# Kernel optimization log

Measured on AMD Instinct MI355X. Metric: run time of the kernel, lower is better.

Reference implementation:

```python
import jax, jax.numpy as jnp
import numpy as np

T, B, H, NH = 256, 64, 768, 12
HD = H // NH


def setup_inputs() -> dict:
    key = jax.random.key(0)
    ks = jax.random.split(key, 24)
    stdv = 1.0 / np.sqrt(H)
    u = lambda k, shape: jax.random.uniform(k, shape, jnp.float32, -stdv, stdv)
    return {
        "question": jax.random.normal(ks[0], (1, B, H), jnp.float32),
        "answer": jax.random.normal(ks[1], (1, B, H), jnp.float32),
        "x": jax.random.normal(ks[2], (T, B, H), jnp.float32),
        "ping": jax.random.randint(ks[3], (B, T), 0, T, jnp.int32),
        "h0": jax.random.normal(ks[4], (1, B, H), jnp.float32),
        "c0": jax.random.normal(ks[5], (1, B, H), jnp.float32),
        # SQACILSTMCell parameters (num_layers=1)
        "Wqh": u(ks[6], (H, 4 * H)), "bqh": u(ks[7], (4 * H,)),
        "Wah": u(ks[8], (H, 4 * H)), "bah": u(ks[9], (4 * H,)),
        "Wih": u(ks[10], (H, 4 * H)), "bih": u(ks[11], (4 * H,)),
        "Whh": u(ks[12], (H, 4 * H)), "bhh": u(ks[13], (4 * H,)),
        # BertSelfAttention parameters
        "Wq": u(ks[14], (H, H)), "bq": u(ks[15], (H,)),
        "Wk": u(ks[16], (H, H)), "bk": u(ks[17], (H,)),
        "Wv": u(ks[18], (H, H)), "bv": u(ks[19], (H,)),
        # fusion linear (ci_mode='all'): Linear(2H -> H), stored as [2H, H]
        "Wfuse": u(ks[20], (2 * H, H)), "bfuse": u(ks[21], (H,)),
    }


def reference(question, answer, x, ping, h0, c0,
              Wqh, bqh, Wah, bah, Wih, bih, Whh, bhh,
              Wq, bq, Wk, bk, Wv, bv, Wfuse, bfuse):
    Tn, Bn, Hn = x.shape
    scale = 1.0 / np.sqrt(HD)
    barange = jnp.arange(Bn)
    # q/a contributions are time-invariant: precompute once
    base = (question[0] @ Wqh + bqh) + (answer[0] @ Wah + bah) + bih + bhh  # [B,4H]

    def attn2(pair):  # pair: [B,2,H] -> fused [B,H]
        def heads(y):
            return y.reshape(Bn, 2, NH, HD).transpose(0, 2, 1, 3)  # [B,NH,2,HD]
        q = heads(pair @ Wq + bq)
        k = heads(pair @ Wk + bk)
        v = heads(pair @ Wv + bv)
        s = jnp.einsum('bhqd,bhkd->bhqk', q, k) * scale
        p = jax.nn.softmax(s, axis=-1)
        ctx = jnp.einsum('bhqk,bhkd->bhqd', p, v).transpose(0, 2, 1, 3).reshape(Bn, 2, Hn)
        # ci_mode='all': concat both tokens then linear 2H->H
        return jnp.concatenate([ctx[:, 0], ctx[:, 1]], axis=-1) @ Wfuse + bfuse

    def step(carry, t):
        h_prev, c_prev, inputs = carry
        pt = ping[:, t]  # [B]
        left = inputs[jnp.clip(pt - 1, 0, Tn - 1), barange]  # [B,H] data-dependent gather
        right = inputs[t]  # [B,H]
        fused = attn2(jnp.stack([left, right], axis=1))
        newv = jnp.where(((pt > 0) & (t > 0))[:, None], fused, right)
        inputs = inputs.at[t].set(newv)  # refactoring persists across steps
        gates = base + newv @ Wih + h_prev @ Whh  # [B,4H]
        i, f, g, o = jnp.split(gates, 4, axis=1)
        c = jax.nn.sigmoid(f) * c_prev + jax.nn.sigmoid(i) * jnp.tanh(g)
        h = jax.nn.sigmoid(o) * jnp.tanh(c)
        return (h, c, inputs), h

    (hT, cT, _), h_all = jax.lax.scan(step, (h0[0], c0[0], x), jnp.arange(Tn))
    # matches torch return: (h[:, -1], (h[-1], c[-1])) with num_layers=1
    return h_all, hT[None], cT[None]
```

## Files before the change

### kernel.cpp

```cpp
#include <hip/hip_runtime.h>
#include <cstdint>
#include <cstddef>


#define T_   256
#define B_   64
#define NBLK 72
#define NTHR 256
#define GRIDTH (NBLK*NTHR)
#define HALL 12582912

typedef __attribute__((ext_vector_type(8))) short short8;
typedef __attribute__((ext_vector_type(4))) float f4;
typedef unsigned long long u64t;
typedef unsigned short u16t;
typedef unsigned int u32t;

struct Params {
  const float* question; const float* answer; const float* x; const int* ping;
  const float* h0; const float* c0;
  const float* Wqh; const float* bqh; const float* Wah; const float* bah;
  const float* Wih; const float* bih; const float* Whh; const float* bhh;
  const float* Wq;  const float* bq;  const float* Wk;  const float* bk;
  const float* Wv;  const float* bv;  const float* Wfuse; const float* bfuse;
  float* out;
  u32t* flags; u32t* gen;
  u16t* Wqkv_s; u16t* Whhih_s; u16t* Wfuse_s; u16t* Wcomb_s; u16t* Wfuse_bf;
  float* base; float* gatesHX; u16t* ctxb; u16t* hB; float* cbuf; float* bfW;
  u16t* xB;
};

__device__ __forceinline__ u16t f2b(float f){
  union { float f; u32t u; } a; a.f = f;
  u32t u = a.u;
  u32t r = u + 0x7FFFu + ((u >> 16) & 1u);
  return (u16t)(r >> 16);
}
__device__ __forceinline__ float b2f(u16t u){
  union { u32t u; float f; } a; a.u = ((u32t)u) << 16; return a.f;
}
__device__ __forceinline__ u64t pack4f(float a, float b, float c, float d){
  return (u64t)f2b(a) | ((u64t)f2b(b)<<16) | ((u64t)f2b(c)<<32) | ((u64t)f2b(d)<<48);
}
__device__ __forceinline__ float sigm(float x){ return 1.0f/(1.0f+__expf(-x)); }
__device__ __forceinline__ float tanh_(float x){ return 2.0f/(1.0f+__expf(-2.0f*x)) - 1.0f; }
__device__ __forceinline__ f4 mfma16(short8 a, short8 b, f4 c){
  return __builtin_amdgcn_mfma_f32_16x16x32_bf16(a, b, c, 0, 0, 0);
}
__device__ __forceinline__ float wsum(float x){
  #pragma unroll
  for (int off = 32; off > 0; off >>= 1) x += __shfl_xor(x, off, 64);
  return x;
}

__device__ __forceinline__ void cldx4_8(f4&d0,f4&d1,f4&d2,f4&d3,f4&d4,f4&d5,f4&d6,f4&d7,
  const void*a0,const void*a1,const void*a2,const void*a3,
  const void*a4,const void*a5,const void*a6,const void*a7){
  asm volatile(
    "global_load_dwordx4 %0, %8, off sc0 sc1\n\t"
    "global_load_dwordx4 %1, %9, off sc0 sc1\n\t"
    "global_load_dwordx4 %2, %10, off sc0 sc1\n\t"
    "global_load_dwordx4 %3, %11, off sc0 sc1\n\t"
    "global_load_dwordx4 %4, %12, off sc0 sc1\n\t"
    "global_load_dwordx4 %5, %13, off sc0 sc1\n\t"
    "global_load_dwordx4 %6, %14, off sc0 sc1\n\t"
    "global_load_dwordx4 %7, %15, off sc0 sc1\n\t"
    "s_waitcnt vmcnt(0)"
    : "=&v"(d0),"=&v"(d1),"=&v"(d2),"=&v"(d3),"=&v"(d4),"=&v"(d5),"=&v"(d6),"=&v"(d7)
    : "v"(a0),"v"(a1),"v"(a2),"v"(a3),"v"(a4),"v"(a5),"v"(a6),"v"(a7));
}
__device__ __forceinline__ void cldx4_4(f4&d0,f4&d1,f4&d2,f4&d3,
  const void*a0,const void*a1,const void*a2,const void*a3){
  asm volatile(
    "global_load_dwordx4 %0, %4, off sc0 sc1\n\t"
    "global_load_dwordx4 %1, %5, off sc0 sc1\n\t"
    "global_load_dwordx4 %2, %6, off sc0 sc1\n\t"
    "global_load_dwordx4 %3, %7, off sc0 sc1\n\t"
    "s_waitcnt vmcnt(0)"
    : "=&v"(d0),"=&v"(d1),"=&v"(d2),"=&v"(d3)
    : "v"(a0),"v"(a1),"v"(a2),"v"(a3));
}
__device__ __forceinline__ void cldd8(float&d0,float&d1,float&d2,float&d3,float&d4,float&d5,float&d6,float&d7,
  const float*a0,const float*a1,const float*a2,const float*a3,
  const float*a4,const float*a5,const float*a6,const float*a7){
  asm volatile(
    "global_load_dword %0, %8, off sc0 sc1\n\t"
    "global_load_dword %1, %9, off sc0 sc1\n\t"
    "global_load_dword %2, %10, off sc0 sc1\n\t"
    "global_load_dword %3, %11, off sc0 sc1\n\t"
    "global_load_dword %4, %12, off sc0 sc1\n\t"
    "global_load_dword %5, %13, off sc0 sc1\n\t"
    "global_load_dword %6, %14, off sc0 sc1\n\t"
    "global_load_dword %7, %15, off sc0 sc1\n\t"
    "s_waitcnt vmcnt(0)"
    : "=&v"(d0),"=&v"(d1),"=&v"(d2),"=&v"(d3),"=&v"(d4),"=&v"(d5),"=&v"(d6),"=&v"(d7)
    : "v"(a0),"v"(a1),"v"(a2),"v"(a3),"v"(a4),"v"(a5),"v"(a6),"v"(a7));
}

__device__ __forceinline__ void cstf(float* p, float v){
  __hip_atomic_store(p, v, __ATOMIC_RELAXED, __HIP_MEMORY_SCOPE_AGENT);
}
__device__ __forceinline__ void cst32(u32t* p, u32t v){
  __hip_atomic_store(p, v, __ATOMIC_RELAXED, __HIP_MEMORY_SCOPE_AGENT);
}

__device__ __forceinline__ void aput16(u16t* As, int rowu16, int m, int cc, f4 v){
  int slot = (cc & ~7) | ((cc ^ m) & 7);
  *(f4*)(As + m*rowu16 + slot*8) = v;
}
__device__ __forceinline__ short8 afrag(const u16t* As, int rowu16, int m, int kb, int q4){
  int c = kb*4 + q4;
  int phys = (c & ~7) | ((c ^ m) & 7);
  return *(const short8*)(As + m*rowu16 + phys*8);
}

__device__ __forceinline__ void gsync(u32t* flags, u32t* gen, u32t e){
  asm volatile("s_waitcnt vmcnt(0) lgkmcnt(0)" ::: "memory");
  __syncthreads();
  if (blockIdx.x == 0){
    if (threadIdx.x > 0 && threadIdx.x < NBLK){
      while (__hip_atomic_load(flags + threadIdx.x*32, __ATOMIC_RELAXED, __HIP_MEMORY_SCOPE_AGENT) < e) ;
    }
    __syncthreads();
    if (threadIdx.x == 0)
      __hip_atomic_store(gen, e, __ATOMIC_RELAXED, __HIP_MEMORY_SCOPE_AGENT);
  } else {
    if (threadIdx.x == 0){
      __hip_atomic_store(flags + blockIdx.x*32, e, __ATOMIC_RELAXED, __HIP_MEMORY_SCOPE_AGENT);
      while (__hip_atomic_load(gen, __ATOMIC_RELAXED, __HIP_MEMORY_SCOPE_AGENT) < e) ;
    }
  }
  __builtin_amdgcn_fence(__ATOMIC_ACQUIRE, "workgroup");
  __syncthreads();
}

__launch_bounds__(NTHR, 1)
__global__ void sqac_kernel(Params p){
  extern __shared__ u16t As[];
  __shared__ u16t qkvs[64*192];
  __shared__ int anyX;
  const int tid0 = threadIdx.x;
  const int blk  = blockIdx.x;
  const int tid  = blk*NTHR + tid0;
  const int lane = tid0 & 63;
  const int wv   = tid0 >> 6;
  const int c16  = lane & 15, q4 = lane >> 4;
  u32t e = 0;

  {
    for (int idx = tid; idx < 12288; idx += GRIDTH){
      f4 h = *(const f4*)(p.h0 + idx*4);
      *(u64t*)(p.hB + idx*4) = pack4f(h.x, h.y, h.z, h.w);
      *(f4*)(p.cbuf + idx*4) = *(const f4*)(p.c0 + idx*4);
    }
    for (int idx = tid; idx < 3145728; idx += GRIDTH){
      f4 v = *(const f4*)(p.x + (size_t)idx*4);
      *(u64t*)(p.xB + (size_t)idx*4) = pack4f(v.x, v.y, v.z, v.w);
    }
    for (int idx = tid; idx < 221184; idx += GRIDTH){
      int l = idx & 63, g2 = idx >> 6;
      int ntl = g2 % 12, kb = (g2/12) % 24, h = g2/288;
      int k0 = kb*32 + ((l>>4)<<3);
      int nl = ntl*16 + (l&15);
      const float* s; int col;
      if (nl < 64){ s = p.Wq; col = h*64 + nl; }
      else if (nl < 128){ s = p.Wk; col = h*64 + nl - 64; }
      else { s = p.Wv; col = h*64 + nl - 128; }
      union { u16t a[8]; short8 v; } t8;
      #pragma unroll
      for (int j = 0; j < 8; j++) t8.a[j] = f2b(s[(size_t)(k0+j)*768 + col]);
      *(short8*)(p.Wqkv_s + (size_t)idx*8) = t8.v;
    }
    for (int idx = tid; idx < 589824; idx += GRIDTH){
      int l = idx & 63, g2 = idx >> 6;
      int nb = g2 % 192, kb2 = g2 / 192;
      int n  = nb*16 + (l&15);
      int kl = (kb2 % 24)*32 + ((l>>4)<<3);
      const float* s = (kb2 < 24) ? p.Whh : p.Wih;
      union { u16t a[8]; short8 v; } t8;
      #pragma unroll
      for (int j = 0; j < 8; j++) t8.a[j] = f2b(s[(size_t)(kl+j)*3072 + n]);
      *(short8*)(p.Whhih_s + (size_t)idx*8) = t8.v;
    }
    for (int idx = tid; idx < 147456; idx += GRIDTH){
      int l = idx & 63, g2 = idx >> 6;
      int nb = g2 % 48, kb = g2 / 48;
      int n  = nb*16 + (l&15);
      int k0 = kb*32 + ((l>>4)<<3);
      union { u16t a[8]; short8 v; } t8;
      #pragma unroll
      for (int j = 0; j < 8; j++) t8.a[j] = f2b(p.Wfuse[(size_t)(k0+j)*768 + n]);
      *(short8*)(p.Wfuse_s + (size_t)idx*8) = t8.v;
    }
    for (int idx = tid; idx < 294912; idx += GRIDTH){
      f4 v = *(const f4*)(p.Wfuse + idx*4);
      *(u64t*)(p.Wfuse_bf + idx*4) = pack4f(v.x, v.y, v.z, v.w);
    }
    for (int w = tid; w < 24576; w += GRIDTH){
      int bg = w / 3072, n = w - bg*3072;
      float acc[8];
      #pragma unroll
      for (int bi = 0; bi < 8; bi++) acc[bi] = 0.f;
      for (int k = 0; k < 768; k++){
        float wq = p.Wqh[(size_t)k*3072 + n];
        float wa = p.Wah[(size_t)k*3072 + n];
        #pragma unroll
        for (int bi = 0; bi < 8; bi++){
          int b = bg*8 + bi;
          acc[bi] += p.question[b*768 + k]*wq + p.answer[b*768 + k]*wa;
        }
      }
      float bias = p.bqh[n] + p.bah[n] + p.bih[n] + p.bhh[n];
      #pragma unroll
      for (int bi = 0; bi < 8; bi++)
        p.base[(size_t)(bg*8+bi)*3072 + n] = acc[bi] + bias;
    }
    for (int n = tid; n < 3072; n += GRIDTH){
      float a = 0.f;
      for (int k = 0; k < 768; k++) a += p.bfuse[k]*p.Wih[(size_t)k*3072 + n];
      p.bfW[n] = a;
    }
  }
  __threadfence();
  e++; gsync(p.flags, p.gen, e);

  {
    int w = tid >> 6;
    int mt = w % 96, ntg = w / 96;
    for (int nt = ntg*64; nt < ntg*64 + 64; nt++){
      f4 acc = {0.f,0.f,0.f,0.f};
      for (int kb = 0; kb < 24; kb++){
        short8 af = *(const short8*)(p.Wfuse_bf + (size_t)(mt*16 + c16)*768 + kb*32 + q4*8);
        short8 bf = *(const short8*)(p.Whhih_s + ((size_t)((24+kb)*192 + nt))*512 + lane*8);
        acc = mfma16(af, bf, acc);
      }
      #pragma unroll
      for (int r = 0; r < 4; r++){
        int k1 = mt*16 + q4*4 + r;
        p.Wcomb_s[((size_t)((k1>>5)*192 + nt))*512 + (size_t)((((k1>>3)&3)*16 + c16)*8 + (k1&7))] = f2b(acc[r]);
      }
    }
  }
  __threadfence();
  e++; gsync(p.flags, p.gen, e);

  for (int t = 0; t < T_; t++){

    if (blk < 24){
      int h, bh;
      if (blk < 16){ h = blk & 7; bh = blk >> 3; }
      else { int l2 = blk - 16; h = 8 + (l2 & 3); bh = l2 >> 2; }
      {
        int m = tid0 >> 2, j = tid0 & 3;
        int b = bh*32 + (m & 31);
        int st;
        if (m < 32){ int pt = p.ping[b*T_ + t]; st = pt - 1; if (st < 0) st = 0; if (st > T_-1) st = T_-1; }
        else st = t;
        const f4* src = (const f4*)(p.xB + ((size_t)(st*64 + b))*768);
        #pragma unroll
        for (int g = 0; g < 3; g++){
          f4 d0,d1,d2,d3,d4,d5,d6,d7;
          int c0 = j + 32*g;
          cldx4_8(d0,d1,d2,d3,d4,d5,d6,d7,
                  src+c0,    src+c0+ 4, src+c0+ 8, src+c0+12,
                  src+c0+16, src+c0+20, src+c0+24, src+c0+28);
          aput16(As,768,m,c0,    d0); aput16(As,768,m,c0+ 4,d1);
          aput16(As,768,m,c0+ 8, d2); aput16(As,768,m,c0+12,d3);
          aput16(As,768,m,c0+16, d4); aput16(As,768,m,c0+20,d5);
          aput16(As,768,m,c0+24, d6); aput16(As,768,m,c0+28,d7);
        }
      }
      __syncthreads();
      f4 acc[3][4];
      #pragma unroll
      for (int i = 0; i < 3; i++)
        #pragma unroll
        for (int mt = 0; mt < 4; mt++) acc[i][mt] = f4{0.f,0.f,0.f,0.f};
      for (int kb = 0; kb < 24; kb++){
        short8 af[4];
        #pragma unroll
        for (int mt = 0; mt < 4; mt++) af[mt] = afrag(As, 768, mt*16 + c16, kb, q4);
        #pragma unroll
        for (int i = 0; i < 3; i++){
          short8 bf = *(const short8*)(p.Wqkv_s + ((size_t)((h*24 + kb)*12 + wv*3 + i))*512 + lane*8);
          #pragma unroll
          for (int mt = 0; mt < 4; mt++) acc[i][mt] = mfma16(af[mt], bf, acc[i][mt]);
        }
      }
      #pragma unroll
      for (int i = 0; i < 3; i++){
        int nl = (wv*3 + i)*16 + c16;
        float bias = (nl < 64) ? p.bq[h*64+nl] : (nl < 128 ? p.bk[h*64+nl-64] : p.bv[h*64+nl-128]);
        #pragma unroll
        for (int mt = 0; mt < 4; mt++)
          #pragma unroll
          for (int r = 0; r < 4; r++)
            qkvs[(mt*16 + q4*4 + r)*192 + nl] = f2b(acc[i][mt][r] + bias);
      }
      __syncthreads();
      for (int pi = 0; pi < 8; pi++){
        int bi = wv*8 + pi;
        const u16t* L = qkvs + bi*192;
        const u16t* R = qkvs + (32+bi)*192;
        float ql = b2f(L[lane]), kl = b2f(L[64+lane]), vl = b2f(L[128+lane]);
        float qr = b2f(R[lane]), kr = b2f(R[64+lane]), vr = b2f(R[128+lane]);
        float sll = wsum(ql*kl)*0.125f, slr = wsum(ql*kr)*0.125f;
        float srl = wsum(qr*kl)*0.125f, srr = wsum(qr*kr)*0.125f;
        float ml = fmaxf(sll, slr), mr = fmaxf(srl, srr);
        float ell = __expf(sll-ml), elr = __expf(slr-ml);
        float erl = __expf(srl-mr), err = __expf(srr-mr);
        float il = 1.0f/(ell+elr), ir = 1.0f/(erl+err);
        float cl = (ell*il)*vl + (elr*il)*vr;
        float cr = (erl*ir)*vl + (err*ir)*vr;
        float cl2 = __shfl_xor(cl, 1), cr2 = __shfl_xor(cr, 1);
        if (!(lane & 1)){
          int b = bh*32 + bi;
          cst32((u32t*)(p.ctxb + (size_t)b*1536 + h*64 + lane),
                (u32t)f2b(cl) | ((u32t)f2b(cl2) << 16));
          cst32((u32t*)(p.ctxb + (size_t)b*1536 + 768 + h*64 + lane),
                (u32t)f2b(cr) | ((u32t)f2b(cr2) << 16));
        }
      }
    } else {
      const int local = blk - 24, mh = local / 24, ng = local % 24;
      const int b0 = mh*32;
      if (tid0 == 0) anyX = 0;
      __syncthreads();
      {
        int m = tid0 >> 3, j = tid0 & 7;
        int b = b0 + m;
        int pt = p.ping[b*T_ + t];
        bool cond = (pt > 0) && (t > 0);
        const f4* hsrc = (const f4*)(p.hB + (size_t)b*768);
        {
          f4 d0,d1,d2,d3,d4,d5,d6,d7;
          cldx4_8(d0,d1,d2,d3,d4,d5,d6,d7,
                  hsrc+j,    hsrc+j+ 8, hsrc+j+16, hsrc+j+24,
                  hsrc+j+32, hsrc+j+40, hsrc+j+48, hsrc+j+56);
          aput16(As,1536,m,j,    d0); aput16(As,1536,m,j+ 8,d1);
          aput16(As,1536,m,j+16, d2); aput16(As,1536,m,j+24,d3);
          aput16(As,1536,m,j+32, d4); aput16(As,1536,m,j+40,d5);
          aput16(As,1536,m,j+48, d6); aput16(As,1536,m,j+56,d7);
          f4 e0,e1,e2,e3;
          cldx4_4(e0,e1,e2,e3, hsrc+j+64, hsrc+j+72, hsrc+j+80, hsrc+j+88);
          aput16(As,1536,m,j+64, e0); aput16(As,1536,m,j+72,e1);
          aput16(As,1536,m,j+80, e2); aput16(As,1536,m,j+88,e3);
        }
        if (cond){
          #pragma unroll
          for (int i = 0; i < 12; i++) aput16(As,1536,m,96 + j + 8*i, f4{0.f,0.f,0.f,0.f});
        } else {
          if (j == 0) anyX = 1;
          const f4* xsrc = (const f4*)(p.xB + ((size_t)(t*64 + b))*768);
          f4 d0,d1,d2,d3,d4,d5,d6,d7;
          cldx4_8(d0,d1,d2,d3,d4,d5,d6,d7,
                  xsrc+j,    xsrc+j+ 8, xsrc+j+16, xsrc+j+24,
                  xsrc+j+32, xsrc+j+40, xsrc+j+48, xsrc+j+56);
          aput16(As,1536,m,96+j,    d0); aput16(As,1536,m,96+j+ 8,d1);
          aput16(As,1536,m,96+j+16, d2); aput16(As,1536,m,96+j+24,d3);
          aput16(As,1536,m,96+j+32, d4); aput16(As,1536,m,96+j+40,d5);
          aput16(As,1536,m,96+j+48, d6); aput16(As,1536,m,96+j+56,d7);
          f4 e0,e1,e2,e3;
          cldx4_4(e0,e1,e2,e3, xsrc+j+64, xsrc+j+72, xsrc+j+80, xsrc+j+88);
          aput16(As,1536,m,96+j+64, e0); aput16(As,1536,m,96+j+72,e1);
          aput16(As,1536,m,96+j+80, e2); aput16(As,1536,m,96+j+88,e3);
        }
      }
      __syncthreads();
      const int kbmax = anyX ? 48 : 24;
      f4 acc[2][2];
      #pragma unroll
      for (int i = 0; i < 2; i++)
        #pragma unroll
        for (int mt = 0; mt < 2; mt++) acc[i][mt] = f4{0.f,0.f,0.f,0.f};
      for (int kb = 0; kb < kbmax; kb++){
        short8 af[2];
        #pragma unroll
        for (int mt = 0; mt < 2; mt++) af[mt] = afrag(As, 1536, mt*16 + c16, kb, q4);
        #pragma unroll
        for (int i = 0; i < 2; i++){
          int nt = ng*8 + wv*2 + i;
          short8 bf = *(const short8*)(p.Whhih_s + ((size_t)(kb*192 + nt))*512 + lane*8);
          #pragma unroll
          for (int mt = 0; mt < 2; mt++) acc[i][mt] = mfma16(af[mt], bf, acc[i][mt]);
        }
      }
      #pragma unroll
      for (int i = 0; i < 2; i++){
        int n = (ng*8 + wv*2 + i)*16 + c16;
        #pragma unroll
        for (int mt = 0; mt < 2; mt++)
          #pragma unroll
          for (int r = 0; r < 4; r++){
            int b = b0 + mt*16 + q4*4 + r;
            cstf(p.gatesHX + (size_t)b*3072 + n, acc[i][mt][r]);
          }
      }
    }
    e++; gsync(p.flags, p.gen, e);

    if (blk < 48){
      const int mh = blk / 24, jjg = blk % 24;
      const int b0 = mh*32;
      {
        int m = tid0 >> 3, j = tid0 & 7;
        const f4* src = (const f4*)(p.ctxb + (size_t)(b0+m)*1536);
        #pragma unroll
        for (int g = 0; g < 3; g++){
          f4 d0,d1,d2,d3,d4,d5,d6,d7;
          int c0 = j + 64*g;
          cldx4_8(d0,d1,d2,d3,d4,d5,d6,d7,
                  src+c0,    src+c0+ 8, src+c0+16, src+c0+24,
                  src+c0+32, src+c0+40, src+c0+48, src+c0+56);
          aput16(As,1536,m,c0,    d0); aput16(As,1536,m,c0+ 8,d1);
          aput16(As,1536,m,c0+16, d2); aput16(As,1536,m,c0+24,d3);
          aput16(As,1536,m,c0+32, d4); aput16(As,1536,m,c0+40,d5);
          aput16(As,1536,m,c0+48, d6); aput16(As,1536,m,c0+56,d7);
        }
      }
      __syncthreads();
      const int jjt = jjg*2 + (wv & 1), mt = wv >> 1;
      const int jj = jjt*16 + c16;
      float gx[16];
      {
        const float* a[16];
        #pragma unroll
        for (int r = 0; r < 4; r++){
          int b = b0 + mt*16 + q4*4 + r;
          size_t g0 = (size_t)b*3072 + jj;
          a[r*4+0] = p.gatesHX + g0;        a[r*4+1] = p.gatesHX + g0 + 768;
          a[r*4+2] = p.gatesHX + g0 + 1536; a[r*4+3] = p.gatesHX + g0 + 2304;
        }
        cldd8(gx[0],gx[1],gx[2],gx[3],gx[4],gx[5],gx[6],gx[7],
              a[0],a[1],a[2],a[3],a[4],a[5],a[6],a[7]);
        cldd8(gx[8],gx[9],gx[10],gx[11],gx[12],gx[13],gx[14],gx[15],
              a[8],a[9],a[10],a[11],a[12],a[13],a[14],a[15]);
      }
      f4 acc[4];
      #pragma unroll
      for (int g = 0; g < 4; g++) acc[g] = f4{0.f,0.f,0.f,0.f};
      for (int kb = 0; kb < 48; kb++){
        short8 af = afrag(As, 1536, mt*16 + c16, kb, q4);
        #pragma unroll
        for (int g = 0; g < 4; g++){
          short8 bf = *(const short8*)(p.Wcomb_s + ((size_t)(kb*192 + g*48 + jjt))*512 + lane*8);
          acc[g] = mfma16(af, bf, acc[g]);
        }
      }
      float bfw[4];
      #pragma unroll
      for (int g = 0; g < 4; g++) bfw[g] = p.bfW[g*768 + jj];
      #pragma unroll
      for (int r = 0; r < 4; r++){
        int b = b0 + mt*16 + q4*4 + r;
        int pt = p.ping[b*T_ + t];
        bool cond = (pt > 0) && (t > 0);
        size_t g0 = (size_t)b*3072 + jj;
        float gi = p.base[g0]      + gx[r*4+0];
        float gf = p.base[g0+768]  + gx[r*4+1];
        float gg = p.base[g0+1536] + gx[r*4+2];
        float go = p.base[g0+2304] + gx[r*4+3];
        if (cond){
          gi += acc[0][r] + bfw[0]; gf += acc[1][r] + bfw[1];
          gg += acc[2][r] + bfw[2]; go += acc[3][r] + bfw[3];
        }
        float co = p.cbuf[b*768 + jj];
        float cn = sigm(gf)*co + sigm(gi)*tanh_(gg);
        float hh = sigm(go)*tanh_(cn);
        p.out[((size_t)(t*64 + b))*768 + jj] = hh;
        p.cbuf[b*768 + jj] = cn;
        float hp = __shfl_xor(hh, 1);
        if (!(c16 & 1))
          cst32((u32t*)(p.hB + (size_t)b*768 + jj), (u32t)f2b(hh) | ((u32t)f2b(hp) << 16));
        if (t == T_-1){
          p.out[HALL + b*768 + jj] = hh;
          p.out[HALL + 49152 + b*768 + jj] = cn;
        }
      }
    } else {
      const int local = blk - 48;
      int ng, mh;
      if (local < 16){ ng = local & 7; mh = local >> 3; }
      else { int l2 = local - 16; ng = 8 + (l2 & 3); mh = l2 >> 2; }
      const int b0 = mh*32;
      {
        int m = tid0 >> 3, j = tid0 & 7;
        const f4* src = (const f4*)(p.ctxb + (size_t)(b0+m)*1536);
        #pragma unroll
        for (int g = 0; g < 3; g++){
          f4 d0,d1,d2,d3,d4,d5,d6,d7;
          int c0 = j + 64*g;
          cldx4_8(d0,d1,d2,d3,d4,d5,d6,d7,
                  src+c0,    src+c0+ 8, src+c0+16, src+c0+24,
                  src+c0+32, src+c0+40, src+c0+48, src+c0+56);
          aput16(As,1536,m,c0,    d0); aput16(As,1536,m,c0+ 8,d1);
          aput16(As,1536,m,c0+16, d2); aput16(As,1536,m,c0+24,d3);
          aput16(As,1536,m,c0+32, d4); aput16(As,1536,m,c0+40,d5);
          aput16(As,1536,m,c0+48, d6); aput16(As,1536,m,c0+56,d7);
        }
      }
      __syncthreads();
      const int nt = ng*4 + wv;
      f4 acc[2];
      #pragma unroll
      for (int mt = 0; mt < 2; mt++) acc[mt] = f4{0.f,0.f,0.f,0.f};
      for (int kb = 0; kb < 48; kb++){
        short8 bf = *(const short8*)(p.Wfuse_s + ((size_t)(kb*48 + nt))*512 + lane*8);
        #pragma unroll
        for (int mt = 0; mt < 2; mt++){
          short8 af = afrag(As, 1536, mt*16 + c16, kb, q4);
          acc[mt] = mfma16(af, bf, acc[mt]);
        }
      }
      const int n = nt*16 + c16;
      const float bias = p.bfuse[n];
      #pragma unroll
      for (int mt = 0; mt < 2; mt++)
        #pragma unroll
        for (int r = 0; r < 4; r++){
          int b = b0 + mt*16 + q4*4 + r;
          int pt = p.ping[b*T_ + t];
          float v = acc[mt][r] + bias;
          float v2 = __shfl_xor(v, 1);
          if ((pt > 0) && (t > 0) && !(c16 & 1))
            cst32((u32t*)(p.xB + ((size_t)(t*64 + b))*768 + n),
                  (u32t)f2b(v) | ((u32t)f2b(v2) << 16));
        }
    }
    e++; gsync(p.flags, p.gen, e);
  }
}

extern "C" void kernel_launch(void* const* d_in, const int* in_sizes, int n_in,
                              void* d_out, int out_size, void* d_ws, size_t ws_size,
                              hipStream_t stream)
{
  (void)in_sizes; (void)n_in; (void)out_size; (void)ws_size;
  char* ws = (char*)d_ws;
  size_t off = 0;
  auto take = [&](size_t bytes)->void*{
    void* ptr = ws + off;
    off += (bytes + 255) & ~(size_t)255;
    return ptr;
  };

  Params p;
  p.question = (const float*)d_in[0];
  p.answer   = (const float*)d_in[1];
  p.x        = (const float*)d_in[2];
  p.ping     = (const int*)d_in[3];
  p.h0  = (const float*)d_in[4];  p.c0  = (const float*)d_in[5];
  p.Wqh = (const float*)d_in[6];  p.bqh = (const float*)d_in[7];
  p.Wah = (const float*)d_in[8];  p.bah = (const float*)d_in[9];
  p.Wih = (const float*)d_in[10]; p.bih = (const float*)d_in[11];
  p.Whh = (const float*)d_in[12]; p.bhh = (const float*)d_in[13];
  p.Wq  = (const float*)d_in[14]; p.bq  = (const float*)d_in[15];
  p.Wk  = (const float*)d_in[16]; p.bk  = (const float*)d_in[17];
  p.Wv  = (const float*)d_in[18]; p.bv  = (const float*)d_in[19];
  p.Wfuse = (const float*)d_in[20]; p.bfuse = (const float*)d_in[21];
  p.out = (float*)d_out;

  u32t* sync = (u32t*)take(16384);
  p.flags = sync;
  p.gen   = sync + 3072;

  p.Wqkv_s   = (u16t*)take((size_t)221184*16);
  p.Whhih_s  = (u16t*)take((size_t)589824*16);
  p.Wfuse_s  = (u16t*)take((size_t)147456*16);
  p.Wcomb_s  = (u16t*)take((size_t)589824*16);
  p.Wfuse_bf = (u16t*)take((size_t)1536*768*2);
  p.base     = (float*)take((size_t)64*3072*4);
  p.gatesHX  = (float*)take((size_t)64*3072*4);
  p.ctxb     = (u16t*)take((size_t)64*1536*2);
  p.hB       = (u16t*)take((size_t)64*768*2);
  p.cbuf     = (float*)take((size_t)64*768*4);
  p.bfW      = (float*)take((size_t)3072*4);
  p.xB       = (u16t*)take((size_t)12582912*2);

  hipFuncSetAttribute(reinterpret_cast<const void*>(sqac_kernel),
                      hipFuncAttributeMaxDynamicSharedMemorySize, 98304);
  hipMemsetAsync(sync, 0, 16384, stream);
  hipLaunchKernelGGL(sqac_kernel, dim3(NBLK), dim3(NTHR), 98304, stream, p);
}
```

Before: 17.11 ms.

## Double threads per block with split-K wave pairs and sleep in grid barrier

Raises the block size from 256 to 512 threads and reassigns the new waves in each phase of the persistent recurrent kernel. The QKV and gates GEMMs split work along M, and the fuse and Wcomb GEMMs split K in half, with partial sums reduced through a new shared-memory buffer. Global-to-LDS staging is rewritten for the wider blocks, and the grid-barrier spin loops now call s_sleep to cut memory polling pressure. The aim is more latency hiding per step on the serial time loop, at the cost of extra block-level syncs, reduction traffic and possible barrier wake-up delay.

```diff
diff --git a/kernel.cpp b/kernel.cpp
--- a/kernel.cpp
+++ b/kernel.cpp
@@ -6,7 +6,7 @@
 #define T_   256
 #define B_   64
 #define NBLK 72
-#define NTHR 256
+#define NTHR 512
 #define GRIDTH (NBLK*NTHR)
 #define HALL 12582912
 
@@ -69,6 +69,20 @@
     : "=&v"(d0),"=&v"(d1),"=&v"(d2),"=&v"(d3),"=&v"(d4),"=&v"(d5),"=&v"(d6),"=&v"(d7)
     : "v"(a0),"v"(a1),"v"(a2),"v"(a3),"v"(a4),"v"(a5),"v"(a6),"v"(a7));
 }
+__device__ __forceinline__ void cldx4_6(f4&d0,f4&d1,f4&d2,f4&d3,f4&d4,f4&d5,
+  const void*a0,const void*a1,const void*a2,const void*a3,
+  const void*a4,const void*a5){
+  asm volatile(
+    "global_load_dwordx4 %0, %6, off sc0 sc1\n\t"
+    "global_load_dwordx4 %1, %7, off sc0 sc1\n\t"
+    "global_load_dwordx4 %2, %8, off sc0 sc1\n\t"
+    "global_load_dwordx4 %3, %9, off sc0 sc1\n\t"
+    "global_load_dwordx4 %4, %10, off sc0 sc1\n\t"
+    "global_load_dwordx4 %5, %11, off sc0 sc1\n\t"
+    "s_waitcnt vmcnt(0)"
+    : "=&v"(d0),"=&v"(d1),"=&v"(d2),"=&v"(d3),"=&v"(d4),"=&v"(d5)
+    : "v"(a0),"v"(a1),"v"(a2),"v"(a3),"v"(a4),"v"(a5));
+}
 __device__ __forceinline__ void cldx4_4(f4&d0,f4&d1,f4&d2,f4&d3,
   const void*a0,const void*a1,const void*a2,const void*a3){
   asm volatile(
@@ -119,7 +133,8 @@
   __syncthreads();
   if (blockIdx.x == 0){
     if (threadIdx.x > 0 && threadIdx.x < NBLK){
-      while (__hip_atomic_load(flags + threadIdx.x*32, __ATOMIC_RELAXED, __HIP_MEMORY_SCOPE_AGENT) < e) ;
+      while (__hip_atomic_load(flags + threadIdx.x*32, __ATOMIC_RELAXED, __HIP_MEMORY_SCOPE_AGENT) < e)
+        __builtin_amdgcn_s_sleep(1);
     }
     __syncthreads();
     if (threadIdx.x == 0)
@@ -127,7 +142,8 @@
   } else {
     if (threadIdx.x == 0){
       __hip_atomic_store(flags + blockIdx.x*32, e, __ATOMIC_RELAXED, __HIP_MEMORY_SCOPE_AGENT);
-      while (__hip_atomic_load(gen, __ATOMIC_RELAXED, __HIP_MEMORY_SCOPE_AGENT) < e) ;
+      while (__hip_atomic_load(gen, __ATOMIC_RELAXED, __HIP_MEMORY_SCOPE_AGENT) < e)
+        __builtin_amdgcn_s_sleep(1);
     }
   }
   __builtin_amdgcn_fence(__ATOMIC_ACQUIRE, "workgroup");
@@ -138,6 +154,7 @@
 __global__ void sqac_kernel(Params p){
   extern __shared__ u16t As[];
   __shared__ u16t qkvs[64*192];
+  __shared__ float red[4][64][16];
   __shared__ int anyX;
   const int tid0 = threadIdx.x;
   const int blk  = blockIdx.x;
@@ -227,7 +244,7 @@
   {
     int w = tid >> 6;
     int mt = w % 96, ntg = w / 96;
-    for (int nt = ntg*64; nt < ntg*64 + 64; nt++){
+    for (int nt = ntg*32; nt < ntg*32 + 32; nt++){
       f4 acc = {0.f,0.f,0.f,0.f};
       for (int kb = 0; kb < 24; kb++){
         short8 af = *(const short8*)(p.Wfuse_bf + (size_t)(mt*16 + c16)*768 + kb*32 + q4*8);
@@ -251,55 +268,59 @@
       if (blk < 16){ h = blk & 7; bh = blk >> 3; }
       else { int l2 = blk - 16; h = 8 + (l2 & 3); bh = l2 >> 2; }
       {
-        int m = tid0 >> 2, j = tid0 & 3;
+        int m = tid0 >> 3, j = tid0 & 7;
         int b = bh*32 + (m & 31);
         int st;
         if (m < 32){ int pt = p.ping[b*T_ + t]; st = pt - 1; if (st < 0) st = 0; if (st > T_-1) st = T_-1; }
         else st = t;
         const f4* src = (const f4*)(p.xB + ((size_t)(st*64 + b))*768);
-        #pragma unroll
-        for (int g = 0; g < 3; g++){
-          f4 d0,d1,d2,d3,d4,d5,d6,d7;
-          int c0 = j + 32*g;
-          cldx4_8(d0,d1,d2,d3,d4,d5,d6,d7,
-                  src+c0,    src+c0+ 4, src+c0+ 8, src+c0+12,
-                  src+c0+16, src+c0+20, src+c0+24, src+c0+28);
-          aput16(As,768,m,c0,    d0); aput16(As,768,m,c0+ 4,d1);
-          aput16(As,768,m,c0+ 8, d2); aput16(As,768,m,c0+12,d3);
-          aput16(As,768,m,c0+16, d4); aput16(As,768,m,c0+20,d5);
-          aput16(As,768,m,c0+24, d6); aput16(As,768,m,c0+28,d7);
-        }
-      }
-      __syncthreads();
-      f4 acc[3][4];
+        f4 d0,d1,d2,d3,d4,d5,d6,d7;
+        cldx4_8(d0,d1,d2,d3,d4,d5,d6,d7,
+                src+j,    src+j+ 8, src+j+16, src+j+24,
+                src+j+32, src+j+40, src+j+48, src+j+56);
+        aput16(As,768,m,j,    d0); aput16(As,768,m,j+ 8,d1);
+        aput16(As,768,m,j+16, d2); aput16(As,768,m,j+24,d3);
+        aput16(As,768,m,j+32, d4); aput16(As,768,m,j+40,d5);
+        aput16(As,768,m,j+48, d6); aput16(As,768,m,j+56,d7);
+        f4 e0,e1,e2,e3;
+        cldx4_4(e0,e1,e2,e3, src+j+64, src+j+72, src+j+80, src+j+88);
+        aput16(As,768,m,j+64, e0); aput16(As,768,m,j+72,e1);
+        aput16(As,768,m,j+80, e2); aput16(As,768,m,j+88,e3);
+      }
+      __syncthreads();
+      const int wvL = wv & 3, mh2 = wv >> 2;
+      f4 acc[3][2];
       #pragma unroll
       for (int i = 0; i < 3; i++)
         #pragma unroll
-        for (int mt = 0; mt < 4; mt++) acc[i][mt] = f4{0.f,0.f,0.f,0.f};
+        for (int mtl = 0; mtl < 2; mtl++) acc[i][mtl] = f4{0.f,0.f,0.f,0.f};
       for (int kb = 0; kb < 24; kb++){
-        short8 af[4];
-        #pragma unroll
-        for (int mt = 0; mt < 4; mt++) af[mt] = afrag(As, 768, mt*16 + c16, kb, q4);
+        short8 af[2];
+        #pragma unroll
+        for (int mtl = 0; mtl < 2; mtl++)
+          af[mtl] = afrag(As, 768, (mh2*2 + mtl)*16 + c16, kb, q4);
         #pragma unroll
         for (int i = 0; i < 3; i++){
-          short8 bf = *(const short8*)(p.Wqkv_s + ((size_t)((h*24 + kb)*12 + wv*3 + i))*512 + lane*8);
-          #pragma unroll
-          for (int mt = 0; mt < 4; mt++) acc[i][mt] = mfma16(af[mt], bf, acc[i][mt]);
+          short8 bf = *(const short8*)(p.Wqkv_s + ((size_t)((h*24 + kb)*12 + wvL*3 + i))*512 + lane*8);
+          #pragma unroll
+          for (int mtl = 0; mtl < 2; mtl++) acc[i][mtl] = mfma16(af[mtl], bf, acc[i][mtl]);
         }
       }
       #pragma unroll
       for (int i = 0; i < 3; i++){
-        int nl = (wv*3 + i)*16 + c16;
+        int nl = (wvL*3 + i)*16 + c16;
         float bias = (nl < 64) ? p.bq[h*64+nl] : (nl < 128 ? p.bk[h*64+nl-64] : p.bv[h*64+nl-128]);
         #pragma unroll
-        for (int mt = 0; mt < 4; mt++)
+        for (int mtl = 0; mtl < 2; mtl++){
+          int mt = mh2*2 + mtl;
           #pragma unroll
           for (int r = 0; r < 4; r++)
-            qkvs[(mt*16 + q4*4 + r)*192 + nl] = f2b(acc[i][mt][r] + bias);
-      }
-      __syncthreads();
-      for (int pi = 0; pi < 8; pi++){
-        int bi = wv*8 + pi;
+            qkvs[(mt*16 + q4*4 + r)*192 + nl] = f2b(acc[i][mtl][r] + bias);
+        }
+      }
+      __syncthreads();
+      for (int pi = 0; pi < 4; pi++){
+        int bi = wv*4 + pi;
         const u16t* L = qkvs + bi*192;
         const u16t* R = qkvs + (32+bi)*192;
         float ql = b2f(L[lane]), kl = b2f(L[64+lane]), vl = b2f(L[128+lane]);
@@ -327,74 +348,56 @@
       if (tid0 == 0) anyX = 0;
       __syncthreads();
       {
-        int m = tid0 >> 3, j = tid0 & 7;
+        int m = tid0 >> 4, j = tid0 & 15;
         int b = b0 + m;
         int pt = p.ping[b*T_ + t];
         bool cond = (pt > 0) && (t > 0);
         const f4* hsrc = (const f4*)(p.hB + (size_t)b*768);
         {
-          f4 d0,d1,d2,d3,d4,d5,d6,d7;
-          cldx4_8(d0,d1,d2,d3,d4,d5,d6,d7,
-                  hsrc+j,    hsrc+j+ 8, hsrc+j+16, hsrc+j+24,
-                  hsrc+j+32, hsrc+j+40, hsrc+j+48, hsrc+j+56);
-          aput16(As,1536,m,j,    d0); aput16(As,1536,m,j+ 8,d1);
-          aput16(As,1536,m,j+16, d2); aput16(As,1536,m,j+24,d3);
-          aput16(As,1536,m,j+32, d4); aput16(As,1536,m,j+40,d5);
-          aput16(As,1536,m,j+48, d6); aput16(As,1536,m,j+56,d7);
-          f4 e0,e1,e2,e3;
-          cldx4_4(e0,e1,e2,e3, hsrc+j+64, hsrc+j+72, hsrc+j+80, hsrc+j+88);
-          aput16(As,1536,m,j+64, e0); aput16(As,1536,m,j+72,e1);
-          aput16(As,1536,m,j+80, e2); aput16(As,1536,m,j+88,e3);
+          f4 d0,d1,d2,d3,d4,d5;
+          cldx4_6(d0,d1,d2,d3,d4,d5,
+                  hsrc+j, hsrc+j+16, hsrc+j+32, hsrc+j+48, hsrc+j+64, hsrc+j+80);
+          aput16(As,1536,m,j,    d0); aput16(As,1536,m,j+16,d1);
+          aput16(As,1536,m,j+32, d2); aput16(As,1536,m,j+48,d3);
+          aput16(As,1536,m,j+64, d4); aput16(As,1536,m,j+80,d5);
         }
         if (cond){
           #pragma unroll
-          for (int i = 0; i < 12; i++) aput16(As,1536,m,96 + j + 8*i, f4{0.f,0.f,0.f,0.f});
+          for (int i = 0; i < 6; i++) aput16(As,1536,m,96 + j + 16*i, f4{0.f,0.f,0.f,0.f});
         } else {
           if (j == 0) anyX = 1;
           const f4* xsrc = (const f4*)(p.xB + ((size_t)(t*64 + b))*768);
-          f4 d0,d1,d2,d3,d4,d5,d6,d7;
-          cldx4_8(d0,d1,d2,d3,d4,d5,d6,d7,
-                  xsrc+j,    xsrc+j+ 8, xsrc+j+16, xsrc+j+24,
-                  xsrc+j+32, xsrc+j+40, xsrc+j+48, xsrc+j+56);
-          aput16(As,1536,m,96+j,    d0); aput16(As,1536,m,96+j+ 8,d1);
-          aput16(As,1536,m,96+j+16, d2); aput16(As,1536,m,96+j+24,d3);
-          aput16(As,1536,m,96+j+32, d4); aput16(As,1536,m,96+j+40,d5);
-          aput16(As,1536,m,96+j+48, d6); aput16(As,1536,m,96+j+56,d7);
-          f4 e0,e1,e2,e3;
-          cldx4_4(e0,e1,e2,e3, xsrc+j+64, xsrc+j+72, xsrc+j+80, xsrc+j+88);
-          aput16(As,1536,m,96+j+64, e0); aput16(As,1536,m,96+j+72,e1);
-          aput16(As,1536,m,96+j+80, e2); aput16(As,1536,m,96+j+88,e3);
+          f4 d0,d1,d2,d3,d4,d5;
+          cldx4_6(d0,d1,d2,d3,d4,d5,
+                  xsrc+j, xsrc+j+16, xsrc+j+32, xsrc+j+48, xsrc+j+64, xsrc+j+80);
+          aput16(As,1536,m,96+j,    d0); aput16(As,1536,m,96+j+16,d1);
+          aput16(As,1536,m,96+j+32, d2); aput16(As,1536,m,96+j+48,d3);
+          aput16(As,1536,m,96+j+64, d4); aput16(As,1536,m,96+j+80,d5);
         }
       }
       __syncthreads();
       const int kbmax = anyX ? 48 : 24;
-      f4 acc[2][2];
-      #pragma unroll
-      for (int i = 0; i < 2; i++)
-        #pragma unroll
-        for (int mt = 0; mt < 2; mt++) acc[i][mt] = f4{0.f,0.f,0.f,0.f};
+      const int wvL = wv & 3, mtw = wv >> 2;
+      f4 acc[2];
+      #pragma unroll
+      for (int i = 0; i < 2; i++) acc[i] = f4{0.f,0.f,0.f,0.f};
       for (int kb = 0; kb < kbmax; kb++){
-        short8 af[2];
-        #pragma unroll
-        for (int mt = 0; mt < 2; mt++) af[mt] = afrag(As, 1536, mt*16 + c16, kb, q4);
+        short8 af = afrag(As, 1536, mtw*16 + c16, kb, q4);
         #pragma unroll
         for (int i = 0; i < 2; i++){
-          int nt = ng*8 + wv*2 + i;
+          int nt = ng*8 + wvL*2 + i;
           short8 bf = *(const short8*)(p.Whhih_s + ((size_t)(kb*192 + nt))*512 + lane*8);
-          #pragma unroll
-          for (int mt = 0; mt < 2; mt++) acc[i][mt] = mfma16(af[mt], bf, acc[i][mt]);
+          acc[i] = mfma16(af, bf, acc[i]);
         }
       }
       #pragma unroll
       for (int i = 0; i < 2; i++){
-        int n = (ng*8 + wv*2 + i)*16 + c16;
-        #pragma unroll
-        for (int mt = 0; mt < 2; mt++)
-          #pragma unroll
-          for (int r = 0; r < 4; r++){
-            int b = b0 + mt*16 + q4*4 + r;
-            cstf(p.gatesHX + (size_t)b*3072 + n, acc[i][mt][r]);
-          }
+        int n = (ng*8 + wvL*2 + i)*16 + c16;
+        #pragma unroll
+        for (int r = 0; r < 4; r++){
+          int b = b0 + mtw*16 + q4*4 + r;
+          cstf(p.gatesHX + (size_t)b*3072 + n, acc[i][r]);
+        }
       }
     }
     e++; gsync(p.flags, p.gen, e);
@@ -403,26 +406,26 @@
       const int mh = blk / 24, jjg = blk % 24;
       const int b0 = mh*32;
       {
-        int m = tid0 >> 3, j = tid0 & 7;
+        int m = tid0 >> 4, j = tid0 & 15;
         const f4* src = (const f4*)(p.ctxb + (size_t)(b0+m)*1536);
-        #pragma unroll
-        for (int g = 0; g < 3; g++){
-          f4 d0,d1,d2,d3,d4,d5,d6,d7;
-          int c0 = j + 64*g;
-          cldx4_8(d0,d1,d2,d3,d4,d5,d6,d7,
-                  src+c0,    src+c0+ 8, src+c0+16, src+c0+24,
-                  src+c0+32, src+c0+40, src+c0+48, src+c0+56);
-          aput16(As,1536,m,c0,    d0); aput16(As,1536,m,c0+ 8,d1);
-          aput16(As,1536,m,c0+16, d2); aput16(As,1536,m,c0+24,d3);
-          aput16(As,1536,m,c0+32, d4); aput16(As,1536,m,c0+40,d5);
-          aput16(As,1536,m,c0+48, d6); aput16(As,1536,m,c0+56,d7);
-        }
-      }
-      __syncthreads();
-      const int jjt = jjg*2 + (wv & 1), mt = wv >> 1;
+        f4 d0,d1,d2,d3,d4,d5,d6,d7;
+        cldx4_8(d0,d1,d2,d3,d4,d5,d6,d7,
+                src+j,    src+j+16, src+j+32, src+j+48,
+                src+j+64, src+j+80, src+j+96, src+j+112);
+        aput16(As,1536,m,j,     d0); aput16(As,1536,m,j+ 16,d1);
+        aput16(As,1536,m,j+32,  d2); aput16(As,1536,m,j+ 48,d3);
+        aput16(As,1536,m,j+64,  d4); aput16(As,1536,m,j+ 80,d5);
+        aput16(As,1536,m,j+96,  d6); aput16(As,1536,m,j+112,d7);
+        f4 e0,e1,e2,e3;
+        cldx4_4(e0,e1,e2,e3, src+j+128, src+j+144, src+j+160, src+j+176);
+        aput16(As,1536,m,j+128, e0); aput16(As,1536,m,j+144,e1);
+        aput16(As,1536,m,j+160, e2); aput16(As,1536,m,j+176,e3);
+      }
+      __syncthreads();
+      const int jjt = jjg*2 + (wv & 1), mt = (wv >> 1) & 1, kh = wv >> 2;
       const int jj = jjt*16 + c16;
       float gx[16];
-      {
+      if (kh == 0){
         const float* a[16];
         #pragma unroll
         for (int r = 0; r < 4; r++){
@@ -439,7 +442,7 @@
       f4 acc[4];
       #pragma unroll
       for (int g = 0; g < 4; g++) acc[g] = f4{0.f,0.f,0.f,0.f};
-      for (int kb = 0; kb < 48; kb++){
+      for (int kb = kh*24; kb < kh*24 + 24; kb++){
         short8 af = afrag(As, 1536, mt*16 + c16, kb, q4);
         #pragma unroll
         for (int g = 0; g < 4; g++){
@@ -447,34 +450,49 @@
           acc[g] = mfma16(af, bf, acc[g]);
         }
       }
-      float bfw[4];
-      #pragma unroll
-      for (int g = 0; g < 4; g++) bfw[g] = p.bfW[g*768 + jj];
-      #pragma unroll
-      for (int r = 0; r < 4; r++){
-        int b = b0 + mt*16 + q4*4 + r;
-        int pt = p.ping[b*T_ + t];
-        bool cond = (pt > 0) && (t > 0);
-        size_t g0 = (size_t)b*3072 + jj;
-        float gi = p.base[g0]      + gx[r*4+0];
-        float gf = p.base[g0+768]  + gx[r*4+1];
-        float gg = p.base[g0+1536] + gx[r*4+2];
-        float go = p.base[g0+2304] + gx[r*4+3];
-        if (cond){
-          gi += acc[0][r] + bfw[0]; gf += acc[1][r] + bfw[1];
-          gg += acc[2][r] + bfw[2]; go += acc[3][r] + bfw[3];
-        }
-        float co = p.cbuf[b*768 + jj];
-        float cn = sigm(gf)*co + sigm(gi)*tanh_(gg);
-        float hh = sigm(go)*tanh_(cn);
-        p.out[((size_t)(t*64 + b))*768 + jj] = hh;
-        p.cbuf[b*768 + jj] = cn;
-        float hp = __shfl_xor(hh, 1);
-        if (!(c16 & 1))
-          cst32((u32t*)(p.hB + (size_t)b*768 + jj), (u32t)f2b(hh) | ((u32t)f2b(hp) << 16));
-        if (t == T_-1){
-          p.out[HALL + b*768 + jj] = hh;
-          p.out[HALL + 49152 + b*768 + jj] = cn;
+      if (kh == 1){
+        #pragma unroll
+        for (int g = 0; g < 4; g++)
+          #pragma unroll
+          for (int r = 0; r < 4; r++)
+            red[wv & 3][lane][g*4 + r] = acc[g][r];
+      }
+      __syncthreads();
+      if (kh == 0){
+        #pragma unroll
+        for (int g = 0; g < 4; g++)
+          #pragma unroll
+          for (int r = 0; r < 4; r++)
+            acc[g][r] += red[wv][lane][g*4 + r];
+        float bfw[4];
+        #pragma unroll
+        for (int g = 0; g < 4; g++) bfw[g] = p.bfW[g*768 + jj];
+        #pragma unroll
+        for (int r = 0; r < 4; r++){
+          int b = b0 + mt*16 + q4*4 + r;
+          int pt = p.ping[b*T_ + t];
+          bool cond = (pt > 0) && (t > 0);
+          size_t g0 = (size_t)b*3072 + jj;
+          float gi = p.base[g0]      + gx[r*4+0];
+          float gf = p.base[g0+768]  + gx[r*4+1];
+          float gg = p.base[g0+1536] + gx[r*4+2];
+          float go = p.base[g0+2304] + gx[r*4+3];
+          if (cond){
+            gi += acc[0][r] + bfw[0]; gf += acc[1][r] + bfw[1];
+            gg += acc[2][r] + bfw[2]; go += acc[3][r] + bfw[3];
+          }
+          float co = p.cbuf[b*768 + jj];
+          float cn = sigm(gf)*co + sigm(gi)*tanh_(gg);
+          float hh = sigm(go)*tanh_(cn);
+          p.out[((size_t)(t*64 + b))*768 + jj] = hh;
+          p.cbuf[b*768 + jj] = cn;
+          float hp = __shfl_xor(hh, 1);
+          if (!(c16 & 1))
+            cst32((u32t*)(p.hB + (size_t)b*768 + jj), (u32t)f2b(hh) | ((u32t)f2b(hp) << 16));
+          if (t == T_-1){
+            p.out[HALL + b*768 + jj] = hh;
+            p.out[HALL + 49152 + b*768 + jj] = cn;
+          }
         }
       }
     } else {
@@ -484,27 +502,28 @@
       else { int l2 = local - 16; ng = 8 + (l2 & 3); mh = l2 >> 2; }
       const int b0 = mh*32;
       {
-        int m = tid0 >> 3, j = tid0 & 7;
+        int m = tid0 >> 4, j = tid0 & 15;
         const f4* src = (const f4*)(p.ctxb + (size_t)(b0+m)*1536);
-        #pragma unroll
-        for (int g = 0; g < 3; g++){
-          f4 d0,d1,d2,d3,d4,d5,d6,d7;
-          int c0 = j + 64*g;
-          cldx4_8(d0,d1,d2,d3,d4,d5,d6,d7,
-                  src+c0,    src+c0+ 8, src+c0+16, src+c0+24,
-                  src+c0+32, src+c0+40, src+c0+48, src+c0+56);
-          aput16(As,1536,m,c0,    d0); aput16(As,1536,m,c0+ 8,d1);
-          aput16(As,1536,m,c0+16, d2); aput16(As,1536,m,c0+24,d3);
-          aput16(As,1536,m,c0+32, d4); aput16(As,1536,m,c0+40,d5);
-          aput16(As,1536,m,c0+48, d6); aput16(As,1536,m,c0+56,d7);
-        }
-      }
-      __syncthreads();
-      const int nt = ng*4 + wv;
+        f4 d0,d1,d2,d3,d4,d5,d6,d7;
+        cldx4_8(d0,d1,d2,d3,d4,d5,d6,d7,
+                src+j,    src+j+16, src+j+32, src+j+48,
+                src+j+64, src+j+80, src+j+96, src+j+112);
+        aput16(As,1536,m,j,     d0); aput16(As,1536,m,j+ 16,d1);
+        aput16(As,1536,m,j+32,  d2); aput16(As,1536,m,j+ 48,d3);
+        aput16(As,1536,m,j+64,  d4); aput16(As,1536,m,j+ 80,d5);
+        aput16(As,1536,m,j+96,  d6); aput16(As,1536,m,j+112,d7);
+        f4 e0,e1,e2,e3;
+        cldx4_4(e0,e1,e2,e3, src+j+128, src+j+144, src+j+160, src+j+176);
+        aput16(As,1536,m,j+128, e0); aput16(As,1536,m,j+144,e1);
+        aput16(As,1536,m,j+160, e2); aput16(As,1536,m,j+176,e3);
+      }
+      __syncthreads();
+      const int wvL = wv & 3, kh = wv >> 2;
+      const int nt = ng*4 + wvL;
       f4 acc[2];
       #pragma unroll
       for (int mt = 0; mt < 2; mt++) acc[mt] = f4{0.f,0.f,0.f,0.f};
-      for (int kb = 0; kb < 48; kb++){
+      for (int kb = kh*24; kb < kh*24 + 24; kb++){
         short8 bf = *(const short8*)(p.Wfuse_s + ((size_t)(kb*48 + nt))*512 + lane*8);
         #pragma unroll
         for (int mt = 0; mt < 2; mt++){
@@ -512,20 +531,35 @@
           acc[mt] = mfma16(af, bf, acc[mt]);
         }
       }
-      const int n = nt*16 + c16;
-      const float bias = p.bfuse[n];
-      #pragma unroll
-      for (int mt = 0; mt < 2; mt++)
-        #pragma unroll
-        for (int r = 0; r < 4; r++){
-          int b = b0 + mt*16 + q4*4 + r;
-          int pt = p.ping[b*T_ + t];
-          float v = acc[mt][r] + bias;
-          float v2 = __shfl_xor(v, 1);
-          if ((pt > 0) && (t > 0) && !(c16 & 1))
-            cst32((u32t*)(p.xB + ((size_t)(t*64 + b))*768 + n),
-                  (u32t)f2b(v) | ((u32t)f2b(v2) << 16));
-        }
+      if (kh == 1){
+        #pragma unroll
+        for (int mt = 0; mt < 2; mt++)
+          #pragma unroll
+          for (int r = 0; r < 4; r++)
+            red[wvL][lane][mt*4 + r] = acc[mt][r];
+      }
+      __syncthreads();
+      if (kh == 0){
+        #pragma unroll
+        for (int mt = 0; mt < 2; mt++)
+          #pragma unroll
+          for (int r = 0; r < 4; r++)
+            acc[mt][r] += red[wv][lane][mt*4 + r];
+        const int n = nt*16 + c16;
+        const float bias = p.bfuse[n];
+        #pragma unroll
+        for (int mt = 0; mt < 2; mt++)
+          #pragma unroll
+          for (int r = 0; r < 4; r++){
+            int b = b0 + mt*16 + q4*4 + r;
+            int pt = p.ping[b*T_ + t];
+            float v = acc[mt][r] + bias;
+            float v2 = __shfl_xor(v, 1);
+            if ((pt > 0) && (t > 0) && !(c16 & 1))
+              cst32((u32t*)(p.xB + ((size_t)(t*64 + b))*768 + n),
+                    (u32t)f2b(v) | ((u32t)f2b(v2) << 16));
+          }
+      }
     }
     e++; gsync(p.flags, p.gen, e);
   }
```

After: 24.42 ms. 1.43x slower.
